# Optimization experiments

Hardware: AMD Instinct MI355X
Metric: run time of the kernel (lower is better)

The kernel has to match this reference:

```python
import jax, jax.numpy as jnp
import numpy as np

EMB, HEADS = 1024, 16
HEAD_DIM = EMB // HEADS


def _linear(x, W, b):
    # torch nn.Linear convention: x @ W.T + b, W: [out, in]
    return jnp.einsum('bse,oe->bso', x, W) + b


def setup_inputs() -> dict:
    key = jax.random.key(0)
    ks = jax.random.split(key, 11)
    B, S = 2, 2048
    sc = 1.0 / np.sqrt(EMB)
    inp = {
        'x': jax.random.normal(ks[0], (B, S, EMB), dtype=jnp.float32),
        'y': jax.random.normal(ks[1], (B, S, EMB), dtype=jnp.float32),
        'mask': jnp.ones((B, S, S), dtype=jnp.int32),
        'Wq': jax.random.normal(ks[2], (EMB, EMB), dtype=jnp.float32) * sc,
        'bq': jax.random.normal(ks[3], (EMB,), dtype=jnp.float32) * sc,
        'Wk': jax.random.normal(ks[4], (EMB, EMB), dtype=jnp.float32) * sc,
        'bk': jax.random.normal(ks[5], (EMB,), dtype=jnp.float32) * sc,
        'Wv': jax.random.normal(ks[6], (EMB, EMB), dtype=jnp.float32) * sc,
        'bv': jax.random.normal(ks[7], (EMB,), dtype=jnp.float32) * sc,
        'Wo': jax.random.normal(ks[8], (EMB, EMB), dtype=jnp.float32) * sc,
        'bo': jax.random.normal(ks[9], (EMB,), dtype=jnp.float32) * sc,
    }
    return inp


def reference(x, y, mask, Wq, bq, Wk, bk, Wv, bv, Wo, bo):
    B, S, _ = x.shape
    q = _linear(x, Wq, bq).reshape(B, S, HEADS, HEAD_DIM).transpose(0, 2, 1, 3)
    k = _linear(y, Wk, bk).reshape(B, -1, HEADS, HEAD_DIM).transpose(0, 2, 1, 3)
    v = _linear(y, Wv, bv).reshape(B, -1, HEADS, HEAD_DIM).transpose(0, 2, 1, 3)
    # scores: [B, H, Sq, Sk]
    score = jnp.einsum('bhqd,bhkd->bhqk', q, k) / jnp.sqrt(jnp.float32(HEAD_DIM))
    # NOTE: original torch code calls score.masked_fill(...) without assignment,
    # so the mask has no effect on the computation (faithfully ignored here).
    weights = jax.nn.softmax(score, axis=-1)
    attn = jnp.einsum('bhqk,bhkd->bhqd', weights, v)
    attn = attn.transpose(0, 2, 1, 3).reshape(B, S, EMB)
    # dropout is identity in eval mode
    return _linear(attn, Wo, bo)
```

## Files before the change

kernel.cpp:

```cpp
#include <hip/hip_runtime.h>
#include <cstdint>
#include <cstddef>

#define BB 2
#define SS 2048
#define EE 1024
#define HH 16
#define DD 64

typedef __attribute__((ext_vector_type(8))) short short8;
typedef __attribute__((ext_vector_type(4))) short shortx4;
typedef __attribute__((ext_vector_type(8))) unsigned short ushort8;
typedef __attribute__((ext_vector_type(4))) unsigned short ush4;
typedef __attribute__((ext_vector_type(4))) float floatx4;

#define MFMA32(a, b, c) __builtin_amdgcn_mfma_f32_16x16x32_bf16((a), (b), (c), 0, 0, 0)
#define MFMA16(a, b, c) __builtin_amdgcn_mfma_f32_16x16x16bf16_1k((a), (b), (c), 0, 0, 0)

#define QSCALE 0.18033688011112042f

#define G2L16(g, l)                                                        \
    __builtin_amdgcn_global_load_lds(                                      \
        (const __attribute__((address_space(1))) void*)(g),                \
        (__attribute__((address_space(3))) void*)(l), 16, 0, 0)

__device__ __forceinline__ unsigned short f2bf(float f) {
    unsigned int u = __float_as_uint(f);
    u += 0x7fffu + ((u >> 16) & 1u);
    return (unsigned short)(u >> 16);
}

__device__ __forceinline__ unsigned int pkbf(float a, float b) {
    return __builtin_amdgcn_perm(__float_as_uint(b) + 0x8000u,
                                 __float_as_uint(a) + 0x8000u, 0x07060302u);
}

__global__ __launch_bounds__(256) void k_cvt(
    const float* __restrict__ x, unsigned short* __restrict__ xb,
    const float* __restrict__ y, unsigned short* __restrict__ yb,
    const float* __restrict__ w0, unsigned short* __restrict__ d0,
    const float* __restrict__ w1, unsigned short* __restrict__ d1,
    const float* __restrict__ w2, unsigned short* __restrict__ d2,
    const float* __restrict__ w3, unsigned short* __restrict__ d3)
{
    const int g = blockIdx.y;
    if (g >= 2 && blockIdx.x >= 256) return;
    const float* s = (g == 0) ? x : (g == 1) ? y : (g == 2) ? w0
                   : (g == 3) ? w1 : (g == 4) ? w2 : w3;
    unsigned short* d = (g == 0) ? xb : (g == 1) ? yb : (g == 2) ? d0
                      : (g == 3) ? d1 : (g == 4) ? d2 : d3;
    const size_t i = ((size_t)blockIdx.x * 256 + threadIdx.x) * 16;
    floatx4 f0 = *(const floatx4*)(s + i);
    floatx4 f1 = *(const floatx4*)(s + i + 4);
    floatx4 f2 = *(const floatx4*)(s + i + 8);
    floatx4 f3 = *(const floatx4*)(s + i + 12);
    ushort8 o0, o1;
#pragma unroll
    for (int j = 0; j < 4; ++j) { o0[j] = f2bf(f0[j]); o0[j + 4] = f2bf(f1[j]); }
#pragma unroll
    for (int j = 0; j < 4; ++j) { o1[j] = f2bf(f2[j]); o1[j + 4] = f2bf(f3[j]); }
    *(ushort8*)(d + i) = o0;
    *(ushort8*)(d + i + 8) = o1;
}

template <int MT, int OMODE>
__device__ __forceinline__ void gemm_body(
    const unsigned short* __restrict__ A, const unsigned short* __restrict__ W,
    const float* __restrict__ bias, void* __restrict__ Cv, float oscale,
    int m0, int n0, unsigned short* As0, unsigned short* As1,
    unsigned short* Bs0, unsigned short* Bs1)
{
    constexpr int K = 1024, N = 1024, LDT = 32;
    constexpr int MFR = MT / 32;
    const int t = threadIdx.x;
    const int lane = t & 63, w = t >> 6;
    const int q = lane >> 4, c = lane & 15;
    const int wm = w & 1, wn = w >> 1;
    const int lr = lane >> 2, lc = (lane & 3) * 8;

    const unsigned short* gA0 = A + (size_t)(m0 + w * (MT / 4) + lr) * K + lc;
    const unsigned short* gA1 = gA0 + 16 * K;
    unsigned short* lA0_0 = As0 + (w * (MT / 4)) * LDT;
    unsigned short* lA0_1 = lA0_0 + 16 * LDT;
    unsigned short* lA1_0 = As1 + (w * (MT / 4)) * LDT;
    unsigned short* lA1_1 = lA1_0 + 16 * LDT;
    const unsigned short* gB0 = W + (size_t)(n0 + w * 32 + lr) * K + lc;
    const unsigned short* gB1 = gB0 + 16 * K;
    unsigned short* lB0_0 = Bs0 + (w * 32) * LDT;
    unsigned short* lB0_1 = lB0_0 + 16 * LDT;
    unsigned short* lB1_0 = Bs1 + (w * 32) * LDT;
    unsigned short* lB1_1 = lB1_0 + 16 * LDT;

    floatx4 acc[MFR][4] = {};

    for (int kt = 0; kt < K; kt += 64) {
        __syncthreads();
        G2L16(gA0 + kt, lA0_0);
        if constexpr (MT == 128) G2L16(gA1 + kt, lA0_1);
        G2L16(gA0 + kt + 32, lA1_0);
        if constexpr (MT == 128) G2L16(gA1 + kt + 32, lA1_1);
        G2L16(gB0 + kt, lB0_0);
        G2L16(gB1 + kt, lB0_1);
        G2L16(gB0 + kt + 32, lB1_0);
        G2L16(gB1 + kt + 32, lB1_1);
        __syncthreads();

        const unsigned short* Ah[2] = {As0, As1};
        const unsigned short* Bh[2] = {Bs0, Bs1};
#pragma unroll
        for (int hf = 0; hf < 2; ++hf) {
            short8 af[MFR], bfr[4];
#pragma unroll
            for (int mi = 0; mi < MFR; ++mi)
                af[mi] = *(const short8*)
                    &Ah[hf][(wm * (MFR * 16) + mi * 16 + c) * LDT + q * 8];
#pragma unroll
            for (int ni = 0; ni < 4; ++ni)
                bfr[ni] = *(const short8*)
                    &Bh[hf][(wn * 64 + ni * 16 + c) * LDT + q * 8];
#pragma unroll
            for (int mi = 0; mi < MFR; ++mi)
#pragma unroll
                for (int ni = 0; ni < 4; ++ni)
                    acc[mi][ni] = MFMA32(af[mi], bfr[ni], acc[mi][ni]);
        }
    }

#pragma unroll
    for (int ni = 0; ni < 4; ++ni) {
        const int col = n0 + wn * 64 + ni * 16 + c;
        const float bv = bias[col];
#pragma unroll
        for (int mi = 0; mi < MFR; ++mi)
#pragma unroll
            for (int r = 0; r < 4; ++r) {
                const int row = m0 + wm * (MFR * 16) + mi * 16 + q * 4 + r;
                const float v = (acc[mi][ni][r] + bv) * oscale;
                if constexpr (OMODE == 0) {
                    ((unsigned short*)Cv)[(size_t)row * N + col] = f2bf(v);
                } else if constexpr (OMODE == 1) {
                    const int b = row >> 11, s = row & 2047;
                    ((unsigned short*)Cv)[((size_t)(b * 1024 + col)) * SS + s] = f2bf(v);
                } else {
                    ((float*)Cv)[(size_t)row * N + col] = v;
                }
            }
    }
}

__global__ __launch_bounds__(256) void k_gemm_qkv(
    const unsigned short* __restrict__ x, const unsigned short* __restrict__ y,
    const unsigned short* __restrict__ Wq, const float* __restrict__ bq,
    const unsigned short* __restrict__ Wk, const float* __restrict__ bk,
    const unsigned short* __restrict__ Wv, const float* __restrict__ bv,
    unsigned short* __restrict__ Q, unsigned short* __restrict__ Ko,
    unsigned short* __restrict__ Vt)
{
    __shared__ __align__(16) unsigned short As0[128 * 32], As1[128 * 32];
    __shared__ __align__(16) unsigned short Bs0[128 * 32], Bs1[128 * 32];
    const int m0 = blockIdx.y * 128;
    const int nt = blockIdx.x;
    const int g = nt >> 3;
    const int n0 = (nt & 7) * 128;
    if (g == 0) {
        gemm_body<128, 0>(x, Wq, bq, Q, QSCALE, m0, n0, As0, As1, Bs0, Bs1);
    } else if (g == 1) {
        gemm_body<128, 0>(y, Wk, bk, Ko, 1.0f, m0, n0, As0, As1, Bs0, Bs1);
    } else {
        gemm_body<128, 1>(y, Wv, bv, Vt, 1.0f, m0, n0, As0, As1, Bs0, Bs1);
    }
}

__global__ __launch_bounds__(256) void k_gemm_out(
    const unsigned short* __restrict__ A, const unsigned short* __restrict__ W,
    const float* __restrict__ bias, float* __restrict__ C)
{
    __shared__ __align__(16) unsigned short As0[64 * 32], As1[64 * 32];
    __shared__ __align__(16) unsigned short Bs0[128 * 32], Bs1[128 * 32];
    gemm_body<64, 2>(A, W, bias, C, 1.0f, blockIdx.y * 64, blockIdx.x * 128,
                     As0, As1, Bs0, Bs1);
}

__global__ __launch_bounds__(512, 4) void k_attn(
    const unsigned short* __restrict__ Q, const unsigned short* __restrict__ K,
    const unsigned short* __restrict__ Vt, unsigned short* __restrict__ O)
{
    constexpr int LDK = 72;
    constexpr int TSZ = 64 * LDK + 64 * 64;
    __shared__ __align__(16) unsigned short smem[2 * 2 * TSZ];
    float* Ob = (float*)smem;

    const int bh = blockIdx.x, qt = blockIdx.y;
    const int b = bh >> 4, h = bh & 15;
    const int t = threadIdx.x, w = t >> 6;
    const int ws = w >> 2;
    const int wq = w & 3;
    const int lane = t & 63, q = lane >> 4, c = lane & 15;

    unsigned short* Sb = smem + ws * (2 * TSZ);

    short8 qb[2][2];
#pragma unroll
    for (int g = 0; g < 2; ++g) {
        const size_t qoff =
            (size_t)(b * SS + qt * 128 + wq * 32 + g * 16 + c) * EE + h * DD + q * 8;
        qb[g][0] = *(const short8*)(Q + qoff);
        qb[g][1] = *(const short8*)(Q + qoff + 32);
    }

    floatx4 o[2][4] = {};
    floatx4 lacc[2] = {};
    const shortx4 ones = {(short)0x3F80, (short)0x3F80, (short)0x3F80, (short)0x3F80};

    const int ts = t & 255;
    const int sr = ts >> 2, sp = (ts & 3) * 16;
    const int vkey = (sr & 15) << 2;
    const unsigned short* Kg =
        K + (size_t)(b * SS + ws * 1024 + sr) * EE + h * DD + sp;
    const unsigned short* Vg =
        Vt + ((size_t)bh * DD + sr) * SS + ws * 1024 + sp;

    {
        const ushort8* gk = (const ushort8*)Kg;
        ushort8 k0 = gk[0], k1 = gk[1];
        const ushort8* gv = (const ushort8*)Vg;
        ushort8 v0 = gv[0], v1 = gv[1];
        unsigned short* Ks = Sb;
        unsigned short* Vs = Sb + 64 * LDK;
        *(ushort8*)&Ks[sr * LDK + sp] = k0;
        *(ushort8*)&Ks[sr * LDK + sp + 8] = k1;
        *(ush4*)&Vs[sr * 64 + ((sp +  0) ^ vkey)] =
            __builtin_shufflevector(v0, v0, 0, 1, 2, 3);
        *(ush4*)&Vs[sr * 64 + ((sp +  4) ^ vkey)] =
            __builtin_shufflevector(v0, v0, 4, 5, 6, 7);
        *(ush4*)&Vs[sr * 64 + ((sp +  8) ^ vkey)] =
            __builtin_shufflevector(v1, v1, 0, 1, 2, 3);
        *(ush4*)&Vs[sr * 64 + ((sp + 12) ^ vkey)] =
            __builtin_shufflevector(v1, v1, 4, 5, 6, 7);
    }

#pragma unroll 2
    for (int it = 0; it < 16; ++it) {
        const unsigned short* Ks = Sb + (it & 1) * TSZ;
        const unsigned short* Vs = Ks + 64 * LDK;
        __syncthreads();

        const int nit = (it + 1) & 15;
        ushort8 pk0, pk1, pv0, pv1;
        {
            const ushort8* gk = (const ushort8*)(Kg + (size_t)nit * 64 * EE);
            pk0 = gk[0]; pk1 = gk[1];
            const ushort8* gv = (const ushort8*)(Vg + nit * 64);
            pv0 = gv[0]; pv1 = gv[1];
        }

#pragma unroll
        for (int tt = 0; tt < 4; ++tt) {
            const short8 ka0 = *(const short8*)&Ks[(tt * 16 + c) * LDK + q * 8];
            const short8 ka1 = *(const short8*)&Ks[(tt * 16 + c) * LDK + 32 + q * 8];
            shortx4 pa[2];
#pragma unroll
            for (int g = 0; g < 2; ++g) {
                floatx4 s = {0.f, 0.f, 0.f, 0.f};
                s = MFMA32(ka0, qb[g][0], s);
                s = MFMA32(ka1, qb[g][1], s);
                union { unsigned int u[2]; shortx4 v; } pk;
                pk.u[0] = pkbf(__builtin_amdgcn_exp2f(s[0]),
                               __builtin_amdgcn_exp2f(s[1]));
                pk.u[1] = pkbf(__builtin_amdgcn_exp2f(s[2]),
                               __builtin_amdgcn_exp2f(s[3]));
                pa[g] = pk.v;
            }
#pragma unroll
            for (int nd = 0; nd < 4; ++nd) {
                const shortx4 vb = *(const shortx4*)
                    &Vs[(nd * 16 + c) * 64 + (((tt * 4 + q) ^ c) << 2)];
                o[0][nd] = MFMA16(pa[0], vb, o[0][nd]);
                o[1][nd] = MFMA16(pa[1], vb, o[1][nd]);
            }
            lacc[0] = MFMA16(pa[0], ones, lacc[0]);
            lacc[1] = MFMA16(pa[1], ones, lacc[1]);
        }

        {
            unsigned short* Kn = Sb + ((it + 1) & 1) * TSZ;
            unsigned short* Vn = Kn + 64 * LDK;
            *(ushort8*)&Kn[sr * LDK + sp] = pk0;
            *(ushort8*)&Kn[sr * LDK + sp + 8] = pk1;
            *(ush4*)&Vn[sr * 64 + ((sp +  0) ^ vkey)] =
                __builtin_shufflevector(pv0, pv0, 0, 1, 2, 3);
            *(ush4*)&Vn[sr * 64 + ((sp +  4) ^ vkey)] =
                __builtin_shufflevector(pv0, pv0, 4, 5, 6, 7);
            *(ush4*)&Vn[sr * 64 + ((sp +  8) ^ vkey)] =
                __builtin_shufflevector(pv1, pv1, 0, 1, 2, 3);
            *(ush4*)&Vn[sr * 64 + ((sp + 12) ^ vkey)] =
                __builtin_shufflevector(pv1, pv1, 4, 5, 6, 7);
        }
    }

    __syncthreads();
    if (ws == 1) {
#pragma unroll
        for (int g = 0; g < 2; ++g) {
#pragma unroll
            for (int nd = 0; nd < 4; ++nd)
#pragma unroll
                for (int r = 0; r < 4; ++r)
                    Ob[(wq * 32 + g * 16 + q * 4 + r) * 66 + nd * 16 + c] =
                        o[g][nd][r];
            if (c == 0) {
#pragma unroll
                for (int r = 0; r < 4; ++r)
                    Ob[(wq * 32 + g * 16 + q * 4 + r) * 66 + 64] = lacc[g][r];
            }
        }
    }
    __syncthreads();
    if (ws == 0) {
#pragma unroll
        for (int g = 0; g < 2; ++g) {
            float linv[4];
#pragma unroll
            for (int r = 0; r < 4; ++r) {
                const int rr = wq * 32 + g * 16 + q * 4 + r;
#pragma unroll
                for (int nd = 0; nd < 4; ++nd)
                    o[g][nd][r] += Ob[rr * 66 + nd * 16 + c];
                linv[r] = __builtin_amdgcn_rcpf(lacc[g][r] + Ob[rr * 66 + 64]);
            }
            const int orow = b * SS + qt * 128 + wq * 32 + g * 16;
#pragma unroll
            for (int nd = 0; nd < 4; ++nd)
#pragma unroll
                for (int r = 0; r < 4; ++r)
                    O[(size_t)(orow + q * 4 + r) * EE + h * DD + nd * 16 + c] =
                        f2bf(o[g][nd][r] * linv[r]);
        }
    }
}

extern "C" void kernel_launch(void* const* d_in, const int* in_sizes, int n_in,
                              void* d_out, int out_size, void* d_ws, size_t ws_size,
                              hipStream_t stream)
{
    const float* x  = (const float*)d_in[0];
    const float* y  = (const float*)d_in[1];
    const float* Wq = (const float*)d_in[3];
    const float* bq = (const float*)d_in[4];
    const float* Wk = (const float*)d_in[5];
    const float* bk = (const float*)d_in[6];
    const float* Wv = (const float*)d_in[7];
    const float* bv = (const float*)d_in[8];
    const float* Wo = (const float*)d_in[9];
    const float* bo = (const float*)d_in[10];
    float* out = (float*)d_out;

    char* ws = (char*)d_ws;
    const size_t SZ = (size_t)BB * SS * EE * sizeof(unsigned short);
    const size_t WZ = (size_t)EE * EE * sizeof(unsigned short);
    unsigned short* xb  = (unsigned short*)(ws);
    unsigned short* yb  = (unsigned short*)(ws + SZ);
    unsigned short* Wqb = (unsigned short*)(ws + 2 * SZ);
    unsigned short* Wkb = (unsigned short*)(ws + 2 * SZ + WZ);
    unsigned short* Wvb = (unsigned short*)(ws + 2 * SZ + 2 * WZ);
    unsigned short* Wob = (unsigned short*)(ws + 2 * SZ + 3 * WZ);
    unsigned short* Qw  = (unsigned short*)(ws + 2 * SZ + 4 * WZ);
    unsigned short* Kw  = (unsigned short*)(ws + 3 * SZ + 4 * WZ);
    unsigned short* Vtw = (unsigned short*)(ws + 4 * SZ + 4 * WZ);
    unsigned short* Aw  = (unsigned short*)(ws + 5 * SZ + 4 * WZ);
    (void)ws_size; (void)in_sizes; (void)n_in; (void)out_size;

    k_cvt<<<dim3(1024, 6), 256, 0, stream>>>(x, xb, y, yb, Wq, Wqb, Wk, Wkb,
                                             Wv, Wvb, Wo, Wob);
    k_gemm_qkv<<<dim3(24, 32), 256, 0, stream>>>(xb, yb, Wqb, bq, Wkb, bk, Wvb, bv,
                                                 Qw, Kw, Vtw);
    k_attn<<<dim3(32, 16), 512, 0, stream>>>(Qw, Kw, Vtw, Aw);
    k_gemm_out<<<dim3(8, 64), 256, 0, stream>>>(Aw, Wob, bo, out);
}
```

Before: 228.7 us.

## Ping-pong GEMM K-halves so global-to-LDS loads overlap MFMA compute

```diff
diff --git a/kernel.cpp b/kernel.cpp
--- a/kernel.cpp
+++ b/kernel.cpp
@@ -80,50 +80,56 @@
 
     const unsigned short* gA0 = A + (size_t)(m0 + w * (MT / 4) + lr) * K + lc;
     const unsigned short* gA1 = gA0 + 16 * K;
-    unsigned short* lA0_0 = As0 + (w * (MT / 4)) * LDT;
-    unsigned short* lA0_1 = lA0_0 + 16 * LDT;
-    unsigned short* lA1_0 = As1 + (w * (MT / 4)) * LDT;
-    unsigned short* lA1_1 = lA1_0 + 16 * LDT;
     const unsigned short* gB0 = W + (size_t)(n0 + w * 32 + lr) * K + lc;
     const unsigned short* gB1 = gB0 + 16 * K;
-    unsigned short* lB0_0 = Bs0 + (w * 32) * LDT;
-    unsigned short* lB0_1 = lB0_0 + 16 * LDT;
-    unsigned short* lB1_0 = Bs1 + (w * 32) * LDT;
-    unsigned short* lB1_1 = lB1_0 + 16 * LDT;
+    unsigned short* lA0 = As0 + (w * (MT / 4)) * LDT;
+    unsigned short* lA1 = As1 + (w * (MT / 4)) * LDT;
+    unsigned short* lB0 = Bs0 + (w * 32) * LDT;
+    unsigned short* lB1 = Bs1 + (w * 32) * LDT;
 
     floatx4 acc[MFR][4] = {};
+
+    auto compute = [&](const unsigned short* Ah, const unsigned short* Bh) {
+        short8 af[MFR], bfr[4];
+#pragma unroll
+        for (int mi = 0; mi < MFR; ++mi)
+            af[mi] = *(const short8*)
+                &Ah[(wm * (MFR * 16) + mi * 16 + c) * LDT + q * 8];
+#pragma unroll
+        for (int ni = 0; ni < 4; ++ni)
+            bfr[ni] = *(const short8*)
+                &Bh[(wn * 64 + ni * 16 + c) * LDT + q * 8];
+#pragma unroll
+        for (int mi = 0; mi < MFR; ++mi)
+#pragma unroll
+            for (int ni = 0; ni < 4; ++ni)
+                acc[mi][ni] = MFMA32(af[mi], bfr[ni], acc[mi][ni]);
+    };
+
+    G2L16(gA0, lA0);
+    if constexpr (MT == 128) G2L16(gA1, lA0 + 16 * LDT);
+    G2L16(gB0, lB0);
+    G2L16(gB1, lB0 + 16 * LDT);
 
     for (int kt = 0; kt < K; kt += 64) {
         __syncthreads();
-        G2L16(gA0 + kt, lA0_0);
-        if constexpr (MT == 128) G2L16(gA1 + kt, lA0_1);
-        G2L16(gA0 + kt + 32, lA1_0);
-        if constexpr (MT == 128) G2L16(gA1 + kt + 32, lA1_1);
-        G2L16(gB0 + kt, lB0_0);
-        G2L16(gB1 + kt, lB0_1);
-        G2L16(gB0 + kt + 32, lB1_0);
-        G2L16(gB1 + kt + 32, lB1_1);
+        {
+            const int nk = kt + 32;
+            G2L16(gA0 + nk, lA1);
+            if constexpr (MT == 128) G2L16(gA1 + nk, lA1 + 16 * LDT);
+            G2L16(gB0 + nk, lB1);
+            G2L16(gB1 + nk, lB1 + 16 * LDT);
+        }
+        compute(As0, Bs0);
         __syncthreads();
-
-        const unsigned short* Ah[2] = {As0, As1};
-        const unsigned short* Bh[2] = {Bs0, Bs1};
-#pragma unroll
-        for (int hf = 0; hf < 2; ++hf) {
-            short8 af[MFR], bfr[4];
-#pragma unroll
-            for (int mi = 0; mi < MFR; ++mi)
-                af[mi] = *(const short8*)
-                    &Ah[hf][(wm * (MFR * 16) + mi * 16 + c) * LDT + q * 8];
-#pragma unroll
-            for (int ni = 0; ni < 4; ++ni)
-                bfr[ni] = *(const short8*)
-                    &Bh[hf][(wn * 64 + ni * 16 + c) * LDT + q * 8];
-#pragma unroll
-            for (int mi = 0; mi < MFR; ++mi)
-#pragma unroll
-                for (int ni = 0; ni < 4; ++ni)
-                    acc[mi][ni] = MFMA32(af[mi], bfr[ni], acc[mi][ni]);
-        }
+        {
+            const int nk = (kt + 64) & (K - 1);
+            G2L16(gA0 + nk, lA0);
+            if constexpr (MT == 128) G2L16(gA1 + nk, lA0 + 16 * LDT);
+            G2L16(gB0 + nk, lB0);
+            G2L16(gB1 + nk, lB0 + 16 * LDT);
+        }
+        compute(As1, Bs1);
     }
 
 #pragma unroll
```

Result: no change. 233.3 us (+2.0%).
